# Performance work log

Hardware: AMD Instinct MI355X
Metric: run time of the kernel (lower is better)

## Reference

```python
import jax, jax.numpy as jnp
import numpy as np

D_MODEL = 768
BATCH = 2
N_CTX = 4096


def setup_inputs() -> dict:
    key = jax.random.key(0)
    k1, k2 = jax.random.split(key)
    x = jax.random.normal(k1, (BATCH, N_CTX, D_MODEL), dtype=jnp.float32)
    # proj: Linear(d_model, 3*d_model, bias=False); torch stores weight as [out, in]
    W_proj = jax.random.normal(k2, (3 * D_MODEL, D_MODEL), dtype=jnp.float32) * (1.0 / np.sqrt(D_MODEL))
    return {"x": x, "W_proj": W_proj}


def reference(x, W_proj):
    d = x.shape[-1]
    n_ctx = x.shape[-2]
    # qkv: [B, S, 3D] = x @ W^T (torch Linear semantics)
    qkv = jnp.einsum("bsd,ed->bse", x, W_proj)
    Q, K, V = jnp.split(qkv, 3, axis=-1)
    # additive causal mask: 0 on/below diagonal, -inf above (1 - 1/tril(ones))
    causal = jnp.tril(jnp.ones((n_ctx, n_ctx), dtype=bool))
    mask = jnp.where(causal, 0.0, -jnp.inf).astype(x.dtype)
    # NOTE: no 1/sqrt(d) scaling in the original module
    scores = jnp.einsum("bqd,bkd->bqk", Q, K) + mask
    attn = jax.nn.softmax(scores, axis=-1)
    out = x + jnp.einsum("bqk,bkd->bqd", attn, V)
    return out
```

## Files before the change

kernel.cpp:

```cpp
#include <hip/hip_runtime.h>
#include <hip/hip_bf16.h>
#include <hip/hip_fp16.h>

typedef _Float16 f16;
typedef _Float16 f16x8 __attribute__((ext_vector_type(8)));
typedef _Float16 f16x4 __attribute__((ext_vector_type(4)));
typedef _Float16 f16x2 __attribute__((ext_vector_type(2)));
typedef float f32x4 __attribute__((ext_vector_type(4)));

#define D_MODEL 768
#define S_CTX   4096
#define NBATCH  2
#define M_TOK   (NBATCH * S_CTX)
#define N3      (3 * D_MODEL)

__device__ __forceinline__ void gload_lds16(const void* g, void* l) {
  __builtin_amdgcn_global_load_lds(
      (__attribute__((address_space(1))) unsigned int*)g,
      (__attribute__((address_space(3))) unsigned int*)l, 16, 0, 0);
}

__global__ __launch_bounds__(256) void cvt_f32_f16(const float* __restrict__ s,
                                                   f16* __restrict__ d, int n4) {
  int i = blockIdx.x * 256 + threadIdx.x;
  if (i >= n4) return;
  f32x4 v = ((const f32x4*)s)[i];
  f16x4 h;
  h[0] = (f16)v[0]; h[1] = (f16)v[1]; h[2] = (f16)v[2]; h[3] = (f16)v[3];
  ((f16x4*)d)[i] = h;
}

__global__ __launch_bounds__(256, 2) void proj_gemm(
    const f16* __restrict__ A, const f16* __restrict__ B,
    f16* __restrict__ qh, f16* __restrict__ kh, f16* __restrict__ vth) {
  __shared__ f16 As[128 * 32];
  __shared__ f16 Bs[128 * 32];

  const int tid  = threadIdx.x;
  const int w    = tid >> 6, lane = tid & 63;
  const int wr   = w >> 1,   wc   = w & 1;
  const int bm0  = blockIdx.x * 128, bn0 = blockIdx.y * 128;
  const int srow = lane >> 2;
  const int scol = (lane & 3) * 8;

  f32x4 acc[4][4] = {};

  const f16* gA = A + (size_t)bm0 * 768;
  const f16* gB = B + (size_t)bn0 * 768;

  for (int kt = 0; kt < 24; ++kt) {
    __syncthreads();
    const int k0 = kt * 32 + scol;
#pragma unroll
    for (int cc = 0; cc < 2; ++cc) {
      int c = w + cc * 4;
      gload_lds16(gA + (size_t)(c * 16 + srow) * 768 + k0, (char*)As + c * 1024);
      gload_lds16(gB + (size_t)(c * 16 + srow) * 768 + k0, (char*)Bs + c * 1024);
    }
    __syncthreads();

    const int fr = lane & 15, fk = (lane >> 4) * 8;
    f16x8 af[4], bf[4];
#pragma unroll
    for (int i = 0; i < 4; ++i)
      af[i] = *(const f16x8*)(As + (wr * 64 + i * 16 + fr) * 32 + fk);
#pragma unroll
    for (int j = 0; j < 4; ++j)
      bf[j] = *(const f16x8*)(Bs + (wc * 64 + j * 16 + fr) * 32 + fk);
#pragma unroll
    for (int i = 0; i < 4; ++i)
#pragma unroll
      for (int j = 0; j < 4; ++j)
        acc[i][j] = __builtin_amdgcn_mfma_f32_16x16x32_f16(af[i], bf[j], acc[i][j], 0, 0, 0);
  }

  const int fr = lane & 15, fq = lane >> 4;
#pragma unroll
  for (int i = 0; i < 4; ++i) {
#pragma unroll
    for (int j = 0; j < 4; ++j) {
      int gn      = bn0 + wc * 64 + j * 16 + fr;
      int gm_base = bm0 + wr * 64 + i * 16 + fq * 4;
      if (gn < 1536) {
        f16* dst = (gn < 768) ? qh : kh;
        int  col = (gn < 768) ? gn : gn - 768;
#pragma unroll
        for (int r = 0; r < 4; ++r)
          dst[(size_t)(gm_base + r) * 768 + col] = (f16)acc[i][j][r];
      } else {
        int d = gn - 1536;
        int bb = gm_base >> 12, s = gm_base & 4095;
        f16x4 h;
        h[0] = (f16)acc[i][j][0]; h[1] = (f16)acc[i][j][1];
        h[2] = (f16)acc[i][j][2]; h[3] = (f16)acc[i][j][3];
        *(f16x4*)(vth + ((size_t)bb * 768 + d) * 4096 + s) = h;
      }
    }
  }
}

#define SM_K0   0
#define SM_K1   49152
#define SM_SS   98304
#define SM_PS   107008
#define SM_M    109056
#define SM_L    109184
#define SM_F    109312
#define SM_SZ   109440

__global__ __launch_bounds__(512, 2) void attn_part(
    const f16* __restrict__ qg, const f16* __restrict__ kg,
    const f16* __restrict__ vt, f16* __restrict__ p0,
    float* __restrict__ p1, float* __restrict__ ml) {
  extern __shared__ __align__(16) char smem[];
  float* Ss0 = (float*)(smem + SM_SS);
  float* Ss1 = Ss0 + 32 * 34;
  char*  Ps  = smem + SM_PS;
  float* mS  = (float*)(smem + SM_M);
  float* lS  = (float*)(smem + SM_L);
  float* fS  = (float*)(smem + SM_F);

  const int tid  = threadIdx.x;
  const int wv   = tid >> 6, lane = tid & 63;
  const int fr   = lane & 15, fq = lane >> 4;
  const int qi   = wv >> 2, ki = (wv >> 1) & 1, dh = wv & 1;

  const int u = blockIdx.x;
  int vv = (u < 256) ? u : (u - 256);
  const int qb = ((u < 256) ? 127 : 63) - (vv >> 2);
  const int b  = (vv >> 1) & 1;
  const int c  = vv & 1;
  const int q0 = qb * 32;
  const int n  = (q0 >> 5) + 1;
  const int n0 = (n + 1) >> 1;
  const int ts = c ? n0 : 0;
  const int te = c ? n : n0;

  const char* kbase = (const char*)(kg + (size_t)b * 4096 * 768);
  const f16*  vbase = vt + (size_t)b * 768 * 4096;
  const f16*  vp0   = vbase + (size_t)(wv * 96 + fr) * 4096 + fq * 8;

  f16x8 qreg[12];
  {
    const f16* qp = qg + ((size_t)b * 4096 + q0 + qi * 16 + fr) * 768 + dh * 384 + fq * 8;
#pragma unroll
    for (int kk = 0; kk < 12; ++kk) qreg[kk] = *(const f16x8*)(qp + kk * 32);
  }

  if (tid < 32) { mS[tid] = -1e30f; lS[tid] = 0.f; }

  f32x4 acc[2][6] = {};

  auto stageK = [&](int t) {
    const char* kb = kbase + (size_t)(t * 32) * 1536;
    char* dst = smem + ((t & 1) ? SM_K1 : SM_K0);
#pragma unroll
    for (int i = 0; i < 6; ++i) {
      int lin = wv * 6144 + i * 1024 + lane * 16;
      int row = lin / 1536, cb = lin - row * 1536;
      gload_lds16(kb + (size_t)row * 1536 + (cb ^ ((row & 7) << 4)),
                  dst + wv * 6144 + i * 1024);
    }
  };

  stageK(ts < te ? ts : 0);
  asm volatile("s_waitcnt vmcnt(0)" ::: "memory");
  __builtin_amdgcn_s_barrier();

  for (int t = ts; t < te; ++t) {
    const int kv0 = t * 32;
    const int tn  = t + 1;

    f16x8 vreg[6];
    {
      const f16* vp = vp0 + kv0;
#pragma unroll
      for (int ct = 0; ct < 6; ++ct)
        vreg[ct] = *(const f16x8*)(vp + (size_t)ct * 16 * 4096);
    }
    stageK(tn);

    {
      const char* kbuf = smem + ((t & 1) ? SM_K1 : SM_K0);
      f32x4 sc = {};
      const int krow = ki * 16 + fr;
      const int kswz = (krow & 7) << 4;
      __builtin_amdgcn_s_setprio(1);
#pragma unroll
      for (int kk = 0; kk < 12; ++kk) {
        int by = krow * 1536 + dh * 768 + kk * 64 + fq * 16;
        f16x8 kf = *(const f16x8*)(kbuf + (by ^ kswz));
        sc = __builtin_amdgcn_mfma_f32_16x16x32_f16(qreg[kk], kf, sc, 0, 0, 0);
      }
      __builtin_amdgcn_s_setprio(0);
      float* sdst = (dh ? Ss1 : Ss0) + (qi * 16 + fq * 4) * 34 + ki * 16 + fr;
#pragma unroll
      for (int r = 0; r < 4; ++r) sdst[r * 34] = sc[r];
    }
    asm volatile("s_waitcnt lgkmcnt(0)" ::: "memory");
    __builtin_amdgcn_s_barrier();

    {
      const int row = tid >> 4, sub = tid & 15;
      const int c0 = sub * 2;
      float a0 = Ss0[row * 34 + c0]     + Ss1[row * 34 + c0];
      float a1 = Ss0[row * 34 + c0 + 1] + Ss1[row * 34 + c0 + 1];
      const int grow = q0 + row;
      if (kv0 + c0     > grow) a0 = -1e30f;
      if (kv0 + c0 + 1 > grow) a1 = -1e30f;
      float mx = fmaxf(a0, a1);
      mx = fmaxf(mx, __shfl_xor(mx, 1));
      mx = fmaxf(mx, __shfl_xor(mx, 2));
      mx = fmaxf(mx, __shfl_xor(mx, 4));
      mx = fmaxf(mx, __shfl_xor(mx, 8));
      float mo = mS[row];
      float mn = fmaxf(mo, mx);
      float p0v = __expf(a0 - mn), p1v = __expf(a1 - mn);
      float sum = p0v + p1v;
      sum += __shfl_xor(sum, 1);
      sum += __shfl_xor(sum, 2);
      sum += __shfl_xor(sum, 4);
      sum += __shfl_xor(sum, 8);
      if (sub == 0) {
        float f = __expf(mo - mn);
        mS[row] = mn; fS[row] = f; lS[row] = lS[row] * f + sum;
      }
      f16x2 ph; ph[0] = (f16)p0v; ph[1] = (f16)p1v;
      int by = row * 64 + sub * 4;
      *(f16x2*)(Ps + (by ^ (((row >> 1) & 3) << 4))) = ph;
    }
    asm volatile("s_waitcnt vmcnt(0) lgkmcnt(0)" ::: "memory");
    __builtin_amdgcn_s_barrier();

    {
      f32x4 f0 = *(const f32x4*)(fS + fq * 4);
      f32x4 f1 = *(const f32x4*)(fS + 16 + fq * 4);
      bool nd = (f0[0] < 1.f) | (f0[1] < 1.f) | (f0[2] < 1.f) | (f0[3] < 1.f) |
                (f1[0] < 1.f) | (f1[1] < 1.f) | (f1[2] < 1.f) | (f1[3] < 1.f);
      if (__any(nd)) {
#pragma unroll
        for (int ct = 0; ct < 6; ++ct)
#pragma unroll
          for (int r = 0; r < 4; ++r) {
            acc[0][ct][r] *= f0[r];
            acc[1][ct][r] *= f1[r];
          }
      }
      int byA0 = (fr * 64 + fq * 16) ^ (((fr >> 1) & 3) << 4);
      int rb = 16 + fr;
      int byA1 = (rb * 64 + fq * 16) ^ (((rb >> 1) & 3) << 4);
      f16x8 pa0 = *(const f16x8*)(Ps + byA0);
      f16x8 pa1 = *(const f16x8*)(Ps + byA1);
      __builtin_amdgcn_s_setprio(1);
#pragma unroll
      for (int ct = 0; ct < 6; ++ct) {
        acc[0][ct] = __builtin_amdgcn_mfma_f32_16x16x32_f16(pa0, vreg[ct], acc[0][ct], 0, 0, 0);
        acc[1][ct] = __builtin_amdgcn_mfma_f32_16x16x32_f16(pa1, vreg[ct], acc[1][ct], 0, 0, 0);
      }
      __builtin_amdgcn_s_setprio(0);
    }
  }

  const size_t obase = (size_t)b * 4096 + q0;
  if (c == 0) {
#pragma unroll
    for (int ct = 0; ct < 6; ++ct) {
      int d = wv * 96 + ct * 16 + fr;
#pragma unroll
      for (int r = 0; r < 4; ++r) {
        p0[(obase + fq * 4 + r) * 768 + d]      = (f16)acc[0][ct][r];
        p0[(obase + 16 + fq * 4 + r) * 768 + d] = (f16)acc[1][ct][r];
      }
    }
  } else {
#pragma unroll
    for (int ct = 0; ct < 6; ++ct) {
      int d = wv * 96 + ct * 16 + fr;
#pragma unroll
      for (int r = 0; r < 4; ++r) {
        p1[(obase + fq * 4 + r) * 768 + d]      = acc[0][ct][r];
        p1[(obase + 16 + fq * 4 + r) * 768 + d] = acc[1][ct][r];
      }
    }
  }
  if (tid < 32) {
    float* mlp = ml + ((size_t)(c * 2 + b) * 4096 + q0 + tid) * 2;
    mlp[0] = mS[tid];
    mlp[1] = lS[tid];
  }
}

__global__ __launch_bounds__(256) void attn_combine(
    const float* __restrict__ x, const f16* __restrict__ p0,
    const float* __restrict__ ml, float* __restrict__ out) {
  int i = blockIdx.x * 256 + threadIdx.x;
  int row = i / 192;
  int b = row >> 12, s = row & 4095;
  const float* m0p = ml + ((size_t)b * 4096 + s) * 2;
  const float* m1p = ml + ((size_t)(2 + b) * 4096 + s) * 2;
  float m0 = m0p[0], l0 = m0p[1];
  float m1 = m1p[0], l1 = m1p[1];
  float m  = fmaxf(m0, m1);
  float f0 = __expf(m0 - m), f1 = __expf(m1 - m);
  float inv = 1.f / (l0 * f0 + l1 * f1);
  f32x4 a1 = ((const f32x4*)out)[i];
  f16x4 a0 = ((const f16x4*)p0)[i];
  f32x4 xv = ((const f32x4*)x)[i];
  f32x4 o;
#pragma unroll
  for (int r = 0; r < 4; ++r)
    o[r] = xv[r] + ((float)a0[r] * f0 + a1[r] * f1) * inv;
  ((f32x4*)out)[i] = o;
}

extern "C" void kernel_launch(void* const* d_in, const int* in_sizes, int n_in,
                              void* d_out, int out_size, void* d_ws, size_t ws_size,
                              hipStream_t stream) {
  const float* x  = (const float*)d_in[0];
  const float* Wp = (const float*)d_in[1];
  float* out = (float*)d_out;

  char* ws = (char*)d_ws;
  f16* x_h  = (f16*)(ws);
  f16* w_h  = (f16*)(ws + 12582912);
  f16* q_h  = (f16*)(ws + 16121856);
  f16* k_h  = (f16*)(ws + 28704768);
  f16* vt_h = (f16*)(ws + 41287680);

  f16*   p0 = x_h;
  float* ml = (float*)w_h;

  hipFuncSetAttribute(reinterpret_cast<const void*>(attn_part),
                      hipFuncAttributeMaxDynamicSharedMemorySize, SM_SZ);

  cvt_f32_f16<<<(M_TOK * D_MODEL) / 1024, 256, 0, stream>>>(x, x_h, (M_TOK * D_MODEL) / 4);
  cvt_f32_f16<<<(N3 * D_MODEL) / 1024, 256, 0, stream>>>(Wp, w_h, (N3 * D_MODEL) / 4);
  proj_gemm<<<dim3(64, 18), 256, 0, stream>>>(x_h, w_h, q_h, k_h, vt_h);
  attn_part<<<512, 512, SM_SZ, stream>>>(q_h, k_h, vt_h, p0, out, ml);
  attn_combine<<<(M_TOK * D_MODEL) / 1024, 256, 0, stream>>>(x, p0, ml, out);
}
```

Baseline: 281.2 us.

## Single-buffer K tiles to fit two attention blocks per CU, with atomic work queue

```diff
diff --git a/kernel.cpp b/kernel.cpp
--- a/kernel.cpp
+++ b/kernel.cpp
@@ -29,6 +29,8 @@
   h[0] = (f16)v[0]; h[1] = (f16)v[1]; h[2] = (f16)v[2]; h[3] = (f16)v[3];
   ((f16x4*)d)[i] = h;
 }
+
+__global__ void zero_ctr(int* c) { *c = 0; }
 
 __global__ __launch_bounds__(256, 2) void proj_gemm(
     const f16* __restrict__ A, const f16* __restrict__ B,
@@ -99,19 +101,19 @@
   }
 }
 
-#define SM_K0   0
-#define SM_K1   49152
-#define SM_SS   98304
-#define SM_PS   107008
-#define SM_M    109056
-#define SM_L    109184
-#define SM_F    109312
-#define SM_SZ   109440
+#define SM_K    0
+#define SM_SS   49152
+#define SM_PS   57856
+#define SM_M    59904
+#define SM_L    60032
+#define SM_F    60160
+#define SM_U    60288
+#define SM_SZ   60416
 
 __global__ __launch_bounds__(512, 2) void attn_part(
     const f16* __restrict__ qg, const f16* __restrict__ kg,
     const f16* __restrict__ vt, f16* __restrict__ p0,
-    float* __restrict__ p1, float* __restrict__ ml) {
+    float* __restrict__ p1, float* __restrict__ ml, int* __restrict__ ctr) {
   extern __shared__ __align__(16) char smem[];
   float* Ss0 = (float*)(smem + SM_SS);
   float* Ss1 = Ss0 + 32 * 34;
@@ -125,11 +127,12 @@
   const int fr   = lane & 15, fq = lane >> 4;
   const int qi   = wv >> 2, ki = (wv >> 1) & 1, dh = wv & 1;
 
-  const int u = blockIdx.x;
-  int vv = (u < 256) ? u : (u - 256);
-  const int qb = ((u < 256) ? 127 : 63) - (vv >> 2);
-  const int b  = (vv >> 1) & 1;
-  const int c  = vv & 1;
+  if (tid == 0) *(int*)(smem + SM_U) = atomicAdd(ctr, 1);
+  __syncthreads();
+  const int v  = *(const int*)(smem + SM_U);
+  const int qb = 127 - (v >> 2);
+  const int b  = (v >> 1) & 1;
+  const int c  = v & 1;
   const int q0 = qb * 32;
   const int n  = (q0 >> 5) + 1;
   const int n0 = (n + 1) >> 1;
@@ -153,13 +156,12 @@
 
   auto stageK = [&](int t) {
     const char* kb = kbase + (size_t)(t * 32) * 1536;
-    char* dst = smem + ((t & 1) ? SM_K1 : SM_K0);
 #pragma unroll
     for (int i = 0; i < 6; ++i) {
       int lin = wv * 6144 + i * 1024 + lane * 16;
       int row = lin / 1536, cb = lin - row * 1536;
       gload_lds16(kb + (size_t)row * 1536 + (cb ^ ((row & 7) << 4)),
-                  dst + wv * 6144 + i * 1024);
+                  smem + SM_K + wv * 6144 + i * 1024);
     }
   };
 
@@ -169,7 +171,6 @@
 
   for (int t = ts; t < te; ++t) {
     const int kv0 = t * 32;
-    const int tn  = t + 1;
 
     f16x8 vreg[6];
     {
@@ -178,10 +179,8 @@
       for (int ct = 0; ct < 6; ++ct)
         vreg[ct] = *(const f16x8*)(vp + (size_t)ct * 16 * 4096);
     }
-    stageK(tn);
 
     {
-      const char* kbuf = smem + ((t & 1) ? SM_K1 : SM_K0);
       f32x4 sc = {};
       const int krow = ki * 16 + fr;
       const int kswz = (krow & 7) << 4;
@@ -189,7 +188,7 @@
 #pragma unroll
       for (int kk = 0; kk < 12; ++kk) {
         int by = krow * 1536 + dh * 768 + kk * 64 + fq * 16;
-        f16x8 kf = *(const f16x8*)(kbuf + (by ^ kswz));
+        f16x8 kf = *(const f16x8*)(smem + SM_K + (by ^ kswz));
         sc = __builtin_amdgcn_mfma_f32_16x16x32_f16(qreg[kk], kf, sc, 0, 0, 0);
       }
       __builtin_amdgcn_s_setprio(0);
@@ -199,6 +198,8 @@
     }
     asm volatile("s_waitcnt lgkmcnt(0)" ::: "memory");
     __builtin_amdgcn_s_barrier();
+
+    stageK(t + 1);
 
     {
       const int row = tid >> 4, sub = tid & 15;
@@ -229,7 +230,7 @@
       int by = row * 64 + sub * 4;
       *(f16x2*)(Ps + (by ^ (((row >> 1) & 3) << 4))) = ph;
     }
-    asm volatile("s_waitcnt vmcnt(0) lgkmcnt(0)" ::: "memory");
+    asm volatile("s_waitcnt lgkmcnt(0)" ::: "memory");
     __builtin_amdgcn_s_barrier();
 
     {
@@ -259,6 +260,8 @@
       }
       __builtin_amdgcn_s_setprio(0);
     }
+    asm volatile("s_waitcnt vmcnt(0) lgkmcnt(0)" ::: "memory");
+    __builtin_amdgcn_s_barrier();
   }
 
   const size_t obase = (size_t)b * 4096 + q0;
@@ -327,8 +330,9 @@
   f16* k_h  = (f16*)(ws + 28704768);
   f16* vt_h = (f16*)(ws + 41287680);
 
-  f16*   p0 = x_h;
-  float* ml = (float*)w_h;
+  f16*   p0  = x_h;
+  float* ml  = (float*)w_h;
+  int*   ctr = (int*)(ws + 12582912 + 262144);
 
   hipFuncSetAttribute(reinterpret_cast<const void*>(attn_part),
                       hipFuncAttributeMaxDynamicSharedMemorySize, SM_SZ);
@@ -336,6 +340,7 @@
   cvt_f32_f16<<<(M_TOK * D_MODEL) / 1024, 256, 0, stream>>>(x, x_h, (M_TOK * D_MODEL) / 4);
   cvt_f32_f16<<<(N3 * D_MODEL) / 1024, 256, 0, stream>>>(Wp, w_h, (N3 * D_MODEL) / 4);
   proj_gemm<<<dim3(64, 18), 256, 0, stream>>>(x_h, w_h, q_h, k_h, vt_h);
-  attn_part<<<512, 512, SM_SZ, stream>>>(q_h, k_h, vt_h, p0, out, ml);
+  zero_ctr<<<1, 1, 0, stream>>>(ctr);
+  attn_part<<<512, 512, SM_SZ, stream>>>(q_h, k_h, vt_h, p0, out, ml, ctr);
   attn_combine<<<(M_TOK * D_MODEL) / 1024, 256, 0, stream>>>(x, p0, ml, out);
 }
```

Measured after the change: 305.5 us. +8.6%, slower.
